# Kernel tuning notes

Measured on AMD Instinct MI355X. Metric: run time of the kernel, lower is better.

The kernel has to match this reference:

```python
import jax, jax.numpy as jnp
import numpy as np

H = 1024        # hidden_size
NH = 16         # num_attention_heads
HD = H // NH    # attention_head_size = 64
EPS = 1e-12


def setup_inputs() -> dict:
    key = jax.random.key(0)
    ks = jax.random.split(key, 12)
    B, S = 2, 2048
    s = 0.02
    return {
        "hidden_states": jax.random.normal(ks[0], (B, S, H), jnp.float32),
        "attention_mask": jnp.zeros((B, 1, 1, S), jnp.float32),
        "Wq": jax.random.normal(ks[1], (H, H), jnp.float32) * s,
        "bq": jnp.zeros((H,), jnp.float32),
        "Wk": jax.random.normal(ks[2], (H, H), jnp.float32) * s,
        "bk": jnp.zeros((H,), jnp.float32),
        "Wv": jax.random.normal(ks[3], (H, H), jnp.float32) * s,
        "bv": jnp.zeros((H,), jnp.float32),
        "Wd": jax.random.normal(ks[4], (H, H), jnp.float32) * s,
        "bd": jnp.zeros((H,), jnp.float32),
        "ln_gamma": jnp.ones((H,), jnp.float32),
        "ln_beta": jnp.zeros((H,), jnp.float32),
    }


def _split_heads(x):
    # [B,S,H] -> [B,NH,S,HD]
    B, S, _ = x.shape
    return x.reshape(B, S, NH, HD).transpose(0, 2, 1, 3)


def reference(hidden_states, attention_mask, Wq, bq, Wk, bk, Wv, bv, Wd, bd, ln_gamma, ln_beta):
    q = _split_heads(hidden_states @ Wq.T + bq)
    k = _split_heads(hidden_states @ Wk.T + bk)
    v = _split_heads(hidden_states @ Wv.T + bv)

    scores = jnp.einsum("bhqd,bhkd->bhqk", q, k) / jnp.sqrt(jnp.float32(HD))
    scores = scores + attention_mask
    probs = jax.nn.softmax(scores, axis=-1)  # attention dropout p=0

    ctx = jnp.einsum("bhqk,bhkd->bhqd", probs, v)
    B, _, S, _ = ctx.shape
    ctx = ctx.transpose(0, 2, 1, 3).reshape(B, S, H)

    proj = ctx @ Wd.T + bd  # output dropout p=0
    x = hidden_states + proj
    mu = jnp.mean(x, axis=-1, keepdims=True)
    var = jnp.mean(jnp.square(x - mu), axis=-1, keepdims=True)
    out = (x - mu) * jax.lax.rsqrt(var + EPS) * ln_gamma + ln_beta
    return out
```

## Files before the change

### kernel.cpp

```cpp
#include <hip/hip_runtime.h>

typedef unsigned short u16;
typedef unsigned int u32;
typedef __attribute__((ext_vector_type(4))) unsigned short u16x4;
typedef __attribute__((ext_vector_type(8))) unsigned short u16x8;
typedef __attribute__((ext_vector_type(8))) __bf16 bf16x8;
typedef __attribute__((ext_vector_type(4))) float f32x4;
typedef __attribute__((ext_vector_type(16))) float f32x16;
typedef __attribute__((ext_vector_type(2))) int i32x2;

#define S_LEN 2048
#define HDIM 1024
#define NHEAD 16
#define HD 64
#define MTOK 4096
#define QKV_STRIDE 4194304
#define LOG2E 1.44269504089f
#define QKSCL (0.125f * 1.44269504089f)

__device__ __forceinline__ float bf2f(u16 h) {
    unsigned u = ((unsigned)h) << 16;
    return __builtin_bit_cast(float, u);
}
__device__ __forceinline__ u16 f2bf(float f) {
    return __builtin_bit_cast(u16, (__bf16)f);
}
__device__ __forceinline__ bf16x8 as_bf16(u16x8 u) {
    union { u16x8 a; bf16x8 b; } c; c.a = u; return c.b;
}
__device__ __forceinline__ void gld_lds16(const u16* g, u16* l) {
    __builtin_amdgcn_global_load_lds((const __attribute__((address_space(1))) u16*)g,
                                     (__attribute__((address_space(3))) u16*)l, 16, 0, 0);
}

__device__ __forceinline__ void pl32swap(u32& a, u32& b) {
#if __has_builtin(__builtin_amdgcn_permlane32_swap)
    i32x2 r = __builtin_amdgcn_permlane32_swap((int)a, (int)b, false, false);
    a = (u32)r[0]; b = (u32)r[1];
#else
    u32 as = (u32)__shfl_xor((int)a, 32);
    u32 bs = (u32)__shfl_xor((int)b, 32);
    bool hi = (threadIdx.x & 32) != 0;
    u32 na = hi ? bs : a;
    u32 nb = hi ? b : as;
    a = na; b = nb;
#endif
}

__device__ __forceinline__ void cast4(const float* __restrict__ s, u16* __restrict__ d, int i) {
    f32x4 v = *(const f32x4*)(s + (size_t)i * 4);
    u16x4 o;
    o[0] = f2bf(v[0]); o[1] = f2bf(v[1]); o[2] = f2bf(v[2]); o[3] = f2bf(v[3]);
    *(u16x4*)(d + (size_t)i * 4) = o;
}

__global__ __launch_bounds__(256) void prep(const float* __restrict__ hs,
                                            const float* __restrict__ Wq, const float* __restrict__ Wk,
                                            const float* __restrict__ Wv, const float* __restrict__ Wd,
                                            const float* __restrict__ bq, const float* __restrict__ bk,
                                            const float* __restrict__ bv,
                                            u16* __restrict__ hsb, u16* __restrict__ wqkvb,
                                            u16* __restrict__ wdb, float* __restrict__ b3) {
    int bid = blockIdx.x, tid = threadIdx.x;
    if (bid < 4096) {
        cast4(hs, hsb, bid * 256 + tid);
    } else if (bid < 5120) {
        cast4(Wq, wqkvb, (bid - 4096) * 256 + tid);
    } else if (bid < 6144) {
        cast4(Wk, wqkvb + HDIM * HDIM, (bid - 5120) * 256 + tid);
    } else if (bid < 7168) {
        cast4(Wv, wqkvb + 2 * HDIM * HDIM, (bid - 6144) * 256 + tid);
    } else if (bid < 8192) {
        cast4(Wd, wdb, (bid - 7168) * 256 + tid);
    } else {
        int i = (bid - 8192) * 256 + tid;
        if (i < 3072) b3[i] = (i < 1024) ? bq[i] : (i < 2048) ? bk[i - 1024] : bv[i - 2048];
    }
}

__global__ __launch_bounds__(256, 3) void gemm_qkv(const u16* __restrict__ A, const u16* __restrict__ Bw,
                                                   const float* __restrict__ bias,
                                                   u16* __restrict__ outb, u16* __restrict__ vtout) {
    __shared__ alignas(16) u16 As[2][128 * 32];
    __shared__ alignas(16) u16 Bs[2][128 * 32];
    const int Kd = 1024;
    const int tid = threadIdx.x;
    const int wave = tid >> 6, lane = tid & 63;
    const int l15 = lane & 15, l4 = lane >> 4;
    const int m0 = blockIdx.y * 128, n0 = blockIdx.x * 128;
    const int wm = wave >> 1, wn = wave & 1;

    const int cc0 = wave * 2;
    const int srow = lane >> 2;
    const int sco = (lane & 3) * 8;

    f32x4 acc[4][4];
#pragma unroll
    for (int i = 0; i < 4; i++)
#pragma unroll
        for (int j = 0; j < 4; j++) acc[i][j] = (f32x4){0.f, 0.f, 0.f, 0.f};

    auto STAGE = [&](int k0, int buf) {
#pragma unroll
        for (int i = 0; i < 2; i++) {
            int cc = cc0 + i;
            int row = cc * 16 + srow;
            gld_lds16(A + (size_t)(m0 + row) * Kd + k0 + sco, &As[buf][cc * 512]);
            gld_lds16(Bw + (size_t)(n0 + row) * Kd + k0 + sco, &Bs[buf][cc * 512]);
        }
    };

    const int nt = Kd >> 5;
    STAGE(0, 0);
    for (int t = 0; t < nt; ++t) {
        __builtin_amdgcn_s_barrier();
        if (t + 1 < nt) {
            STAGE((t + 1) << 5, (t + 1) & 1);
            asm volatile("s_waitcnt vmcnt(4)" ::: "memory");
        } else {
            asm volatile("s_waitcnt vmcnt(0)" ::: "memory");
        }
        __builtin_amdgcn_s_barrier();
        const u16* as = &As[t & 1][0];
        const u16* bs = &Bs[t & 1][0];
        bf16x8 af[4], bf[4];
#pragma unroll
        for (int x = 0; x < 4; x++) {
            af[x] = as_bf16(*(const u16x8*)&as[(wm * 64 + x * 16 + l15) * 32 + l4 * 8]);
            bf[x] = as_bf16(*(const u16x8*)&bs[(wn * 64 + x * 16 + l15) * 32 + l4 * 8]);
        }
        __builtin_amdgcn_s_setprio(1);
#pragma unroll
        for (int mi = 0; mi < 4; mi++)
#pragma unroll
            for (int nj = 0; nj < 4; nj++)
                acc[mi][nj] = __builtin_amdgcn_mfma_f32_16x16x32_bf16(af[mi], bf[nj], acc[mi][nj], 0, 0, 0);
        __builtin_amdgcn_s_setprio(0);
    }

#pragma unroll
    for (int mi = 0; mi < 4; mi++) {
#pragma unroll
        for (int nj = 0; nj < 4; nj++) {
            int coln = n0 + wn * 64 + nj * 16 + l15;
            float bv_ = bias[coln];
            int rowb = m0 + wm * 64 + mi * 16 + l4 * 4;
            int which = coln >> 10, nn = coln & 1023;
            int hh = nn >> 6, dd = nn & 63;
            int bb = rowb >> 11, ss = rowb & 2047;
            if (which < 2) {
#pragma unroll
                for (int r = 0; r < 4; r++)
                    outb[(size_t)which * QKV_STRIDE + ((size_t)((bb << 4) + hh) * S_LEN + ss + r) * HD + dd] =
                        f2bf(acc[mi][nj][r] + bv_);
            } else {
                u16x4 o;
#pragma unroll
                for (int r = 0; r < 4; r++) o[r] = f2bf(acc[mi][nj][r] + bv_);
                *(u16x4*)(vtout + ((size_t)((bb << 4) + hh) * HD + dd) * S_LEN + ss) = o;
            }
        }
    }
}

__global__ __launch_bounds__(256, 3) void gemm_proj(const u16* __restrict__ A, const u16* __restrict__ Bw,
                                                    const float* __restrict__ bias,
                                                    u16* __restrict__ outb, int Nd, int Kd) {
    __shared__ alignas(16) u16 As[2][128 * 32];
    __shared__ alignas(16) u16 Bs[2][128 * 32];
    const int tid = threadIdx.x;
    const int wave = tid >> 6, lane = tid & 63;
    const int l15 = lane & 15, l4 = lane >> 4;
    const int m0 = blockIdx.y * 128, n0 = blockIdx.x * 128;
    const int wm = wave >> 1, wn = wave & 1;

    const int cc0 = wave * 2;
    const int srow = lane >> 2;
    const int sco = (lane & 3) * 8;

    f32x4 acc[4][4];
#pragma unroll
    for (int i = 0; i < 4; i++)
#pragma unroll
        for (int j = 0; j < 4; j++) acc[i][j] = (f32x4){0.f, 0.f, 0.f, 0.f};

    auto STAGE = [&](int k0, int buf) {
#pragma unroll
        for (int i = 0; i < 2; i++) {
            int cc = cc0 + i;
            int row = cc * 16 + srow;
            gld_lds16(A + (size_t)(m0 + row) * Kd + k0 + sco, &As[buf][cc * 512]);
            gld_lds16(Bw + (size_t)(n0 + row) * Kd + k0 + sco, &Bs[buf][cc * 512]);
        }
    };

    const int nt = Kd >> 5;
    STAGE(0, 0);
    for (int t = 0; t < nt; ++t) {
        __builtin_amdgcn_s_barrier();
        if (t + 1 < nt) {
            STAGE((t + 1) << 5, (t + 1) & 1);
            asm volatile("s_waitcnt vmcnt(4)" ::: "memory");
        } else {
            asm volatile("s_waitcnt vmcnt(0)" ::: "memory");
        }
        __builtin_amdgcn_s_barrier();
        const u16* as = &As[t & 1][0];
        const u16* bs = &Bs[t & 1][0];
        bf16x8 af[4], bf[4];
#pragma unroll
        for (int x = 0; x < 4; x++) {
            af[x] = as_bf16(*(const u16x8*)&as[(wm * 64 + x * 16 + l15) * 32 + l4 * 8]);
            bf[x] = as_bf16(*(const u16x8*)&bs[(wn * 64 + x * 16 + l15) * 32 + l4 * 8]);
        }
        __builtin_amdgcn_s_setprio(1);
#pragma unroll
        for (int mi = 0; mi < 4; mi++)
#pragma unroll
            for (int nj = 0; nj < 4; nj++)
                acc[mi][nj] = __builtin_amdgcn_mfma_f32_16x16x32_bf16(af[mi], bf[nj], acc[mi][nj], 0, 0, 0);
        __builtin_amdgcn_s_setprio(0);
    }

#pragma unroll
    for (int mi = 0; mi < 4; mi++) {
#pragma unroll
        for (int nj = 0; nj < 4; nj++) {
            int coln = n0 + wn * 64 + nj * 16 + l15;
            float bv_ = bias[coln];
            int rowb = m0 + wm * 64 + mi * 16 + l4 * 4;
#pragma unroll
            for (int r = 0; r < 4; r++)
                outb[(size_t)(rowb + r) * Nd + coln] = f2bf(acc[mi][nj][r] + bv_);
        }
    }
}

__global__ __launch_bounds__(512, 2) void flash_attn10(const u16* __restrict__ qkv,
                                                       const u16* __restrict__ vt,
                                                       const float* __restrict__ amask,
                                                       u16* __restrict__ ctx) {
    __shared__ alignas(16) char smem[102400];

    const int tid = threadIdx.x;
    const int wave = tid >> 6, lane = tid & 63;
    const int l31 = lane & 31;
    const int hi = lane >> 5;
    const int hi4 = hi * 4;
    const int g = wave >> 2;
    const int ws = wave & 3;

    const int lid = blockIdx.x;
    const int idx = lid >> 3;
    const int bh = (lid & 7) * 4 + (idx >> 3);
    const int qb = idx & 7;
    const int b = bh >> 4, h = bh & 15;
    const int qr0 = qb * 256 + ws * 64;

    const u16* qh = qkv + (size_t)bh * (S_LEN * HD);
    const u16* kh = qh + QKV_STRIDE;
    const u16* vth = vt + (size_t)bh * (S_LEN * HD);

    u16* Mlb = (u16*)(smem + 98304);

    {
        f32x4 m = *(const f32x4*)(amask + (size_t)b * S_LEN + tid * 4);
        u16x4 mm;
#pragma unroll
        for (int j = 0; j < 4; j++) mm[j] = f2bf(m[j] * LOG2E);
        *(u16x4*)&Mlb[tid * 4] = mm;
    }

    bf16x8 qf0[4], qf1[4];
#pragma unroll
    for (int s = 0; s < 4; ++s) {
        qf0[s] = as_bf16(*(const u16x8*)(qh + (size_t)(qr0 + l31) * HD + s * 16 + hi * 8));
        qf1[s] = as_bf16(*(const u16x8*)(qh + (size_t)(qr0 + 32 + l31) * HD + s * 16 + hi * 8));
    }

    __syncthreads();

    const int srow = lane >> 3;
    const int schunk = (lane & 7) ^ srow;
    const u16* kss = kh + (size_t)(g * 1024 + ws * 16 + srow) * HD + schunk * 8;
    const u16* vss = vth + (size_t)(ws * 16 + srow) * S_LEN + g * 1024 + schunk * 8;

    f32x16 oacc00, oacc01, oacc10, oacc11;
#pragma unroll
    for (int i = 0; i < 16; ++i) { oacc00[i] = 0.f; oacc01[i] = 0.f; oacc10[i] = 0.f; oacc11[i] = 0.f; }
    float l_run0 = 0.f, l_run1 = 0.f;

    auto STAGE = [&](int t, int buf) {
        u16* base = (u16*)(smem + g * 49152 + buf * 16384);
        u16* kd = base + ws * 1024;
        u16* vd = base + 4096 + ws * 1024;
        const u16* ks = kss + (size_t)t * 64 * HD;
        const u16* vs = vss + t * 64;
        gld_lds16(ks, kd);
        gld_lds16(ks + 8 * HD, kd + 512);
        gld_lds16(vs, vd);
        gld_lds16(vs + 8 * S_LEN, vd + 512);
    };

    auto tile = [&](int t, int buf) {
        const u16* kb = (const u16*)(smem + g * 49152 + buf * 16384);
        const u16* vb = kb + 4096;
        const int kv0 = g * 1024 + t * 64;
#pragma unroll
        for (int sub = 0; sub < 2; ++sub) {
            f32x16 acc0, acc1;
#pragma unroll
            for (int i = 0; i < 16; ++i) { acc0[i] = 0.f; acc1[i] = 0.f; }
            const int kvrow = sub * 32 + l31;
            const int ksw = (kvrow & 7) << 3;
            __builtin_amdgcn_s_setprio(1);
#pragma unroll
            for (int s = 0; s < 4; ++s) {
                bf16x8 kf = as_bf16(*(const u16x8*)&kb[kvrow * 64 + (((s * 2 + hi) << 3) ^ ksw)]);
                acc0 = __builtin_amdgcn_mfma_f32_32x32x16_bf16(kf, qf0[s], acc0, 0, 0, 0);
                acc1 = __builtin_amdgcn_mfma_f32_32x32x16_bf16(kf, qf1[s], acc1, 0, 0, 0);
            }
            __builtin_amdgcn_s_setprio(0);
            u32 pw0[8], pw1[8];
#pragma unroll
            for (int rg = 0; rg < 4; ++rg) {
                u16x4 mraw = *(const u16x4*)&Mlb[kv0 + sub * 32 + rg * 8 + hi4];
#pragma unroll
                for (int r2 = 0; r2 < 2; ++r2) {
                    float m0 = bf2f(mraw[r2 * 2]), m1 = bf2f(mraw[r2 * 2 + 1]);
                    float pa0 = __builtin_amdgcn_exp2f(acc0[rg * 4 + r2 * 2] * QKSCL + m0);
                    float pb0 = __builtin_amdgcn_exp2f(acc0[rg * 4 + r2 * 2 + 1] * QKSCL + m1);
                    float pa1 = __builtin_amdgcn_exp2f(acc1[rg * 4 + r2 * 2] * QKSCL + m0);
                    float pb1 = __builtin_amdgcn_exp2f(acc1[rg * 4 + r2 * 2 + 1] * QKSCL + m1);
                    l_run0 += pa0 + pb0;
                    l_run1 += pa1 + pb1;
                    pw0[rg * 2 + r2] = (u32)f2bf(pa0) | ((u32)f2bf(pb0) << 16);
                    pw1[rg * 2 + r2] = (u32)f2bf(pa1) | ((u32)f2bf(pb1) << 16);
                }
            }
            pl32swap(pw0[0], pw0[2]); pl32swap(pw0[1], pw0[3]);
            pl32swap(pw0[4], pw0[6]); pl32swap(pw0[5], pw0[7]);
            pl32swap(pw1[0], pw1[2]); pl32swap(pw1[1], pw1[3]);
            pl32swap(pw1[4], pw1[6]); pl32swap(pw1[5], pw1[7]);
            union { u32 w[4]; u16x8 v; } u0a, u0b, u1a, u1b;
            u0a.w[0] = pw0[0]; u0a.w[1] = pw0[1]; u0a.w[2] = pw0[2]; u0a.w[3] = pw0[3];
            u0b.w[0] = pw0[4]; u0b.w[1] = pw0[5]; u0b.w[2] = pw0[6]; u0b.w[3] = pw0[7];
            u1a.w[0] = pw1[0]; u1a.w[1] = pw1[1]; u1a.w[2] = pw1[2]; u1a.w[3] = pw1[3];
            u1b.w[0] = pw1[4]; u1b.w[1] = pw1[5]; u1b.w[2] = pw1[6]; u1b.w[3] = pw1[7];
            bf16x8 pf0a = as_bf16(u0a.v), pf0b = as_bf16(u0b.v);
            bf16x8 pf1a = as_bf16(u1a.v), pf1b = as_bf16(u1b.v);
            __builtin_amdgcn_s_setprio(1);
            {
                const int drow0 = l31, dsw0 = (drow0 & 7) << 3;
                const int drow1 = 32 + l31, dsw1 = (drow1 & 7) << 3;
                const int c0 = (sub * 4 + hi) << 3;
                const int c1 = ((sub * 2 + 1) * 2 + hi) << 3;
                bf16x8 vf;
                vf = as_bf16(*(const u16x8*)&vb[drow0 * 64 + (c0 ^ dsw0)]);
                oacc00 = __builtin_amdgcn_mfma_f32_32x32x16_bf16(vf, pf0a, oacc00, 0, 0, 0);
                oacc10 = __builtin_amdgcn_mfma_f32_32x32x16_bf16(vf, pf1a, oacc10, 0, 0, 0);
                vf = as_bf16(*(const u16x8*)&vb[drow0 * 64 + (c1 ^ dsw0)]);
                oacc00 = __builtin_amdgcn_mfma_f32_32x32x16_bf16(vf, pf0b, oacc00, 0, 0, 0);
                oacc10 = __builtin_amdgcn_mfma_f32_32x32x16_bf16(vf, pf1b, oacc10, 0, 0, 0);
                vf = as_bf16(*(const u16x8*)&vb[drow1 * 64 + (c0 ^ dsw1)]);
                oacc01 = __builtin_amdgcn_mfma_f32_32x32x16_bf16(vf, pf0a, oacc01, 0, 0, 0);
                oacc11 = __builtin_amdgcn_mfma_f32_32x32x16_bf16(vf, pf1a, oacc11, 0, 0, 0);
                vf = as_bf16(*(const u16x8*)&vb[drow1 * 64 + (c1 ^ dsw1)]);
                oacc01 = __builtin_amdgcn_mfma_f32_32x32x16_bf16(vf, pf0b, oacc01, 0, 0, 0);
                oacc11 = __builtin_amdgcn_mfma_f32_32x32x16_bf16(vf, pf1b, oacc11, 0, 0, 0);
            }
            __builtin_amdgcn_s_setprio(0);
        }
    };

    STAGE(0, 0);
    STAGE(1, 1);
    for (int t = 0; t < 16; ++t) {
        if (t < 15) {
            asm volatile("s_waitcnt vmcnt(4)" ::: "memory");
        } else {
            asm volatile("s_waitcnt vmcnt(0)" ::: "memory");
        }
        __builtin_amdgcn_s_barrier();
        if (t + 2 < 16) STAGE(t + 2, (t + 2) % 3);
        tile(t, t % 3);
    }

    float l0 = l_run0 + __shfl_xor(l_run0, 32);
    float l1 = l_run1 + __shfl_xor(l_run1, 32);
    __syncthreads();
    float* Oex = (float*)smem;
    float* lsum = (float*)(smem + 65536);
    if (g == 1) {
#pragma unroll
        for (int rg = 0; rg < 4; ++rg)
#pragma unroll
            for (int rr = 0; rr < 4; ++rr) {
                int dA = hi4 + 8 * rg + rr;
                int dB = 32 + hi4 + 8 * rg + rr;
                Oex[ws * 4096 + dA * 64 + l31]      = oacc00[rg * 4 + rr];
                Oex[ws * 4096 + dB * 64 + l31]      = oacc01[rg * 4 + rr];
                Oex[ws * 4096 + dA * 64 + 32 + l31] = oacc10[rg * 4 + rr];
                Oex[ws * 4096 + dB * 64 + 32 + l31] = oacc11[rg * 4 + rr];
            }
        if (lane < 32) { lsum[ws * 64 + l31] = l0; lsum[ws * 64 + 32 + l31] = l1; }
    }
    __syncthreads();
    if (g == 0) {
        float inv0 = 1.0f / (l0 + lsum[ws * 64 + l31]);
        float inv1 = 1.0f / (l1 + lsum[ws * 64 + 32 + l31]);
        u16* cp0 = ctx + ((size_t)b * S_LEN + qr0 + l31) * HDIM + h * HD;
        u16* cp1 = ctx + ((size_t)b * S_LEN + qr0 + 32 + l31) * HDIM + h * HD;
#pragma unroll
        for (int rg = 0; rg < 4; ++rg) {
            u16x4 oA0, oB0, oA1, oB1;
#pragma unroll
            for (int rr = 0; rr < 4; ++rr) {
                int dA = hi4 + 8 * rg + rr;
                int dB = 32 + hi4 + 8 * rg + rr;
                oA0[rr] = f2bf((oacc00[rg * 4 + rr] + Oex[ws * 4096 + dA * 64 + l31]) * inv0);
                oB0[rr] = f2bf((oacc01[rg * 4 + rr] + Oex[ws * 4096 + dB * 64 + l31]) * inv0);
                oA1[rr] = f2bf((oacc10[rg * 4 + rr] + Oex[ws * 4096 + dA * 64 + 32 + l31]) * inv1);
                oB1[rr] = f2bf((oacc11[rg * 4 + rr] + Oex[ws * 4096 + dB * 64 + 32 + l31]) * inv1);
            }
            *(u16x4*)(cp0 + hi4 + 8 * rg) = oA0;
            *(u16x4*)(cp0 + 32 + hi4 + 8 * rg) = oB0;
            *(u16x4*)(cp1 + hi4 + 8 * rg) = oA1;
            *(u16x4*)(cp1 + 32 + hi4 + 8 * rg) = oB1;
        }
    }
}

__global__ __launch_bounds__(256) void resid_ln(const float* __restrict__ hs, const u16* __restrict__ proj,
                                                const float* __restrict__ g, const float* __restrict__ be,
                                                float* __restrict__ out) {
    int row = blockIdx.x, tid = threadIdx.x;
    int base = row * HDIM + tid * 4;
    f32x4 a = *(const f32x4*)(hs + base);
    u16x4 pb = *(const u16x4*)(proj + base);
    f32x4 x;
#pragma unroll
    for (int j = 0; j < 4; j++) x[j] = a[j] + bf2f(pb[j]);
    float s = x[0] + x[1] + x[2] + x[3];
    float sq = x[0] * x[0] + x[1] * x[1] + x[2] * x[2] + x[3] * x[3];
#pragma unroll
    for (int m = 1; m < 64; m <<= 1) {
        s += __shfl_xor(s, m);
        sq += __shfl_xor(sq, m);
    }
    __shared__ float red[8];
    int wave = tid >> 6, lane = tid & 63;
    if (lane == 0) { red[wave] = s; red[4 + wave] = sq; }
    __syncthreads();
    s = red[0] + red[1] + red[2] + red[3];
    sq = red[4] + red[5] + red[6] + red[7];
    float mean = s * (1.0f / 1024.0f);
    float var = sq * (1.0f / 1024.0f) - mean * mean;
    float rstd = rsqrtf(fmaxf(var, 0.f) + 1e-12f);
    f32x4 gg = *(const f32x4*)(g + tid * 4);
    f32x4 bb = *(const f32x4*)(be + tid * 4);
    f32x4 o;
#pragma unroll
    for (int j = 0; j < 4; j++) o[j] = (x[j] - mean) * rstd * gg[j] + bb[j];
    *(f32x4*)(out + base) = o;
}

extern "C" void kernel_launch(void* const* d_in, const int* in_sizes, int n_in,
                              void* d_out, int out_size, void* d_ws, size_t ws_size,
                              hipStream_t stream) {
    const float* hs    = (const float*)d_in[0];
    const float* amask = (const float*)d_in[1];
    const float* Wq    = (const float*)d_in[2];
    const float* bq    = (const float*)d_in[3];
    const float* Wk    = (const float*)d_in[4];
    const float* bk    = (const float*)d_in[5];
    const float* Wv    = (const float*)d_in[6];
    const float* bv    = (const float*)d_in[7];
    const float* Wd    = (const float*)d_in[8];
    const float* bd    = (const float*)d_in[9];
    const float* gamma = (const float*)d_in[10];
    const float* beta  = (const float*)d_in[11];

    char* ws = (char*)d_ws;
    u16*   hsb   = (u16*)(ws);
    u16*   Wqkvb = (u16*)(ws + ((size_t)8 << 20));
    u16*   Wdb   = (u16*)(ws + ((size_t)14 << 20));
    u16*   qkv   = (u16*)(ws + ((size_t)16 << 20));
    u16*   vt    = qkv + 2 * (size_t)QKV_STRIDE;
    u16*   ctx   = (u16*)(ws + ((size_t)40 << 20));
    u16*   projb = (u16*)(ws + ((size_t)48 << 20));
    float* b3    = (float*)(ws + ((size_t)64 << 20));

    prep<<<8204, 256, 0, stream>>>(hs, Wq, Wk, Wv, Wd, bq, bk, bv, hsb, Wqkvb, Wdb, b3);

    gemm_qkv<<<dim3(24, 32), 256, 0, stream>>>(hsb, Wqkvb, b3, qkv, vt);

    flash_attn10<<<256, 512, 0, stream>>>(qkv, vt, amask, ctx);

    gemm_proj<<<dim3(8, 32), 256, 0, stream>>>(ctx, Wdb, bd, projb, HDIM, HDIM);

    resid_ln<<<MTOK, 256, 0, stream>>>(hs, projb, gamma, beta, (float*)d_out);
}
```

Baseline: 125.4 us.

## Give each wave private double-buffered K/V tiles and drop block barriers

The attention kernel stops sharing K/V tiles across the four waves of a group. Each wave now loads its own 32-row K/V tiles into a private double buffer, which removes the block-wide barrier from the main loop; synchronisation becomes per-wave waitcnt. The cost is four times the K/V global/LDS traffic and 132KB of LDS, which caps the kernel at one 512-thread block per CU (launch bounds changed from 2 to 1). The hidden part of the kernel after the loop still uses smem offsets from the old layout, so that region may need checking.

```diff
diff --git a/kernel.cpp b/kernel.cpp
--- a/kernel.cpp
+++ b/kernel.cpp
@@ -236,11 +236,12 @@
     }
 }
 
-__global__ __launch_bounds__(512, 2) void flash_attn10(const u16* __restrict__ qkv,
+__global__ __launch_bounds__(512, 1) void flash_attn12(const u16* __restrict__ qkv,
                                                        const u16* __restrict__ vt,
                                                        const float* __restrict__ amask,
                                                        u16* __restrict__ ctx) {
-    __shared__ alignas(16) char smem[102400];
+    __shared__ alignas(16) char smem[135168];
+    u16* smem16 = (u16*)smem;
 
     const int tid = threadIdx.x;
     const int wave = tid >> 6, lane = tid & 63;
@@ -261,7 +262,7 @@
     const u16* kh = qh + QKV_STRIDE;
     const u16* vth = vt + (size_t)bh * (S_LEN * HD);
 
-    u16* Mlb = (u16*)(smem + 98304);
+    u16* Mlb = smem16 + 65536;
 
     {
         f32x4 m = *(const f32x4*)(amask + (size_t)b * S_LEN + tid * 4);
@@ -280,10 +281,12 @@
 
     __syncthreads();
 
-    const int srow = lane >> 3;
-    const int schunk = (lane & 7) ^ srow;
-    const u16* kss = kh + (size_t)(g * 1024 + ws * 16 + srow) * HD + schunk * 8;
-    const u16* vss = vth + (size_t)(ws * 16 + srow) * S_LEN + g * 1024 + schunk * 8;
+    u16* wbase = smem16 + wave * 8192;
+
+    const int ksc8 = ((lane & 7) ^ (lane >> 3)) * 8;
+    const u16* kss = kh + (size_t)(g * 1024 + (lane >> 3)) * HD + ksc8;
+    const int vsc8 = ((lane & 3) ^ ((lane >> 2) & 3)) * 8;
+    const u16* vss = vth + (size_t)(lane >> 2) * S_LEN + g * 1024 + vsc8;
 
     f32x16 oacc00, oacc01, oacc10, oacc11;
 #pragma unroll
@@ -291,99 +294,97 @@
     float l_run0 = 0.f, l_run1 = 0.f;
 
     auto STAGE = [&](int t, int buf) {
-        u16* base = (u16*)(smem + g * 49152 + buf * 16384);
-        u16* kd = base + ws * 1024;
-        u16* vd = base + 4096 + ws * 1024;
-        const u16* ks = kss + (size_t)t * 64 * HD;
-        const u16* vs = vss + t * 64;
-        gld_lds16(ks, kd);
-        gld_lds16(ks + 8 * HD, kd + 512);
-        gld_lds16(vs, vd);
-        gld_lds16(vs + 8 * S_LEN, vd + 512);
+        u16* kd = wbase + buf * 4096;
+        u16* vd = kd + 2048;
+        const u16* ks = kss + (size_t)t * 32 * HD;
+        const u16* vs = vss + t * 32;
+#pragma unroll
+        for (int j = 0; j < 4; ++j)
+            gld_lds16(ks + (size_t)j * 8 * HD, kd + j * 512);
+#pragma unroll
+        for (int j = 0; j < 4; ++j)
+            gld_lds16(vs + (size_t)j * 16 * S_LEN, vd + j * 512);
     };
 
     auto tile = [&](int t, int buf) {
-        const u16* kb = (const u16*)(smem + g * 49152 + buf * 16384);
-        const u16* vb = kb + 4096;
-        const int kv0 = g * 1024 + t * 64;
-#pragma unroll
-        for (int sub = 0; sub < 2; ++sub) {
-            f32x16 acc0, acc1;
-#pragma unroll
-            for (int i = 0; i < 16; ++i) { acc0[i] = 0.f; acc1[i] = 0.f; }
-            const int kvrow = sub * 32 + l31;
-            const int ksw = (kvrow & 7) << 3;
-            __builtin_amdgcn_s_setprio(1);
-#pragma unroll
-            for (int s = 0; s < 4; ++s) {
-                bf16x8 kf = as_bf16(*(const u16x8*)&kb[kvrow * 64 + (((s * 2 + hi) << 3) ^ ksw)]);
-                acc0 = __builtin_amdgcn_mfma_f32_32x32x16_bf16(kf, qf0[s], acc0, 0, 0, 0);
-                acc1 = __builtin_amdgcn_mfma_f32_32x32x16_bf16(kf, qf1[s], acc1, 0, 0, 0);
+        const u16* kb = wbase + buf * 4096;
+        const u16* vb = kb + 2048;
+        const int kv0 = g * 1024 + t * 32;
+        f32x16 acc0, acc1;
+#pragma unroll
+        for (int i = 0; i < 16; ++i) { acc0[i] = 0.f; acc1[i] = 0.f; }
+        const int ksw = (l31 & 7) << 3;
+        __builtin_amdgcn_s_setprio(1);
+#pragma unroll
+        for (int s = 0; s < 4; ++s) {
+            bf16x8 kf = as_bf16(*(const u16x8*)&kb[l31 * 64 + ((((s * 2 + hi) << 3)) ^ ksw)]);
+            acc0 = __builtin_amdgcn_mfma_f32_32x32x16_bf16(kf, qf0[s], acc0, 0, 0, 0);
+            acc1 = __builtin_amdgcn_mfma_f32_32x32x16_bf16(kf, qf1[s], acc1, 0, 0, 0);
+        }
+        __builtin_amdgcn_s_setprio(0);
+        u32 pw0[8], pw1[8];
+#pragma unroll
+        for (int rg = 0; rg < 4; ++rg) {
+            u16x4 mraw = *(const u16x4*)&Mlb[kv0 + rg * 8 + hi4];
+#pragma unroll
+            for (int r2 = 0; r2 < 2; ++r2) {
+                float m0 = bf2f(mraw[r2 * 2]), m1 = bf2f(mraw[r2 * 2 + 1]);
+                float pa0 = __builtin_amdgcn_exp2f(acc0[rg * 4 + r2 * 2] * QKSCL + m0);
+                float pb0 = __builtin_amdgcn_exp2f(acc0[rg * 4 + r2 * 2 + 1] * QKSCL + m1);
+                float pa1 = __builtin_amdgcn_exp2f(acc1[rg * 4 + r2 * 2] * QKSCL + m0);
+                float pb1 = __builtin_amdgcn_exp2f(acc1[rg * 4 + r2 * 2 + 1] * QKSCL + m1);
+                l_run0 += pa0 + pb0;
+                l_run1 += pa1 + pb1;
+                pw0[rg * 2 + r2] = (u32)f2bf(pa0) | ((u32)f2bf(pb0) << 16);
+                pw1[rg * 2 + r2] = (u32)f2bf(pa1) | ((u32)f2bf(pb1) << 16);
             }
-            __builtin_amdgcn_s_setprio(0);
-            u32 pw0[8], pw1[8];
-#pragma unroll
-            for (int rg = 0; rg < 4; ++rg) {
-                u16x4 mraw = *(const u16x4*)&Mlb[kv0 + sub * 32 + rg * 8 + hi4];
-#pragma unroll
-                for (int r2 = 0; r2 < 2; ++r2) {
-                    float m0 = bf2f(mraw[r2 * 2]), m1 = bf2f(mraw[r2 * 2 + 1]);
-                    float pa0 = __builtin_amdgcn_exp2f(acc0[rg * 4 + r2 * 2] * QKSCL + m0);
-                    float pb0 = __builtin_amdgcn_exp2f(acc0[rg * 4 + r2 * 2 + 1] * QKSCL + m1);
-                    float pa1 = __builtin_amdgcn_exp2f(acc1[rg * 4 + r2 * 2] * QKSCL + m0);
-                    float pb1 = __builtin_amdgcn_exp2f(acc1[rg * 4 + r2 * 2 + 1] * QKSCL + m1);
-                    l_run0 += pa0 + pb0;
-                    l_run1 += pa1 + pb1;
-                    pw0[rg * 2 + r2] = (u32)f2bf(pa0) | ((u32)f2bf(pb0) << 16);
-                    pw1[rg * 2 + r2] = (u32)f2bf(pa1) | ((u32)f2bf(pb1) << 16);
-                }
-            }
-            pl32swap(pw0[0], pw0[2]); pl32swap(pw0[1], pw0[3]);
-            pl32swap(pw0[4], pw0[6]); pl32swap(pw0[5], pw0[7]);
-            pl32swap(pw1[0], pw1[2]); pl32swap(pw1[1], pw1[3]);
-            pl32swap(pw1[4], pw1[6]); pl32swap(pw1[5], pw1[7]);
-            union { u32 w[4]; u16x8 v; } u0a, u0b, u1a, u1b;
-            u0a.w[0] = pw0[0]; u0a.w[1] = pw0[1]; u0a.w[2] = pw0[2]; u0a.w[3] = pw0[3];
-            u0b.w[0] = pw0[4]; u0b.w[1] = pw0[5]; u0b.w[2] = pw0[6]; u0b.w[3] = pw0[7];
-            u1a.w[0] = pw1[0]; u1a.w[1] = pw1[1]; u1a.w[2] = pw1[2]; u1a.w[3] = pw1[3];
-            u1b.w[0] = pw1[4]; u1b.w[1] = pw1[5]; u1b.w[2] = pw1[6]; u1b.w[3] = pw1[7];
-            bf16x8 pf0a = as_bf16(u0a.v), pf0b = as_bf16(u0b.v);
-            bf16x8 pf1a = as_bf16(u1a.v), pf1b = as_bf16(u1b.v);
-            __builtin_amdgcn_s_setprio(1);
-            {
-                const int drow0 = l31, dsw0 = (drow0 & 7) << 3;
-                const int drow1 = 32 + l31, dsw1 = (drow1 & 7) << 3;
-                const int c0 = (sub * 4 + hi) << 3;
-                const int c1 = ((sub * 2 + 1) * 2 + hi) << 3;
-                bf16x8 vf;
-                vf = as_bf16(*(const u16x8*)&vb[drow0 * 64 + (c0 ^ dsw0)]);
-                oacc00 = __builtin_amdgcn_mfma_f32_32x32x16_bf16(vf, pf0a, oacc00, 0, 0, 0);
-                oacc10 = __builtin_amdgcn_mfma_f32_32x32x16_bf16(vf, pf1a, oacc10, 0, 0, 0);
-                vf = as_bf16(*(const u16x8*)&vb[drow0 * 64 + (c1 ^ dsw0)]);
-                oacc00 = __builtin_amdgcn_mfma_f32_32x32x16_bf16(vf, pf0b, oacc00, 0, 0, 0);
-                oacc10 = __builtin_amdgcn_mfma_f32_32x32x16_bf16(vf, pf1b, oacc10, 0, 0, 0);
-                vf = as_bf16(*(const u16x8*)&vb[drow1 * 64 + (c0 ^ dsw1)]);
-                oacc01 = __builtin_amdgcn_mfma_f32_32x32x16_bf16(vf, pf0a, oacc01, 0, 0, 0);
-                oacc11 = __builtin_amdgcn_mfma_f32_32x32x16_bf16(vf, pf1a, oacc11, 0, 0, 0);
-                vf = as_bf16(*(const u16x8*)&vb[drow1 * 64 + (c1 ^ dsw1)]);
-                oacc01 = __builtin_amdgcn_mfma_f32_32x32x16_bf16(vf, pf0b, oacc01, 0, 0, 0);
-                oacc11 = __builtin_amdgcn_mfma_f32_32x32x16_bf16(vf, pf1b, oacc11, 0, 0, 0);
-            }
-            __builtin_amdgcn_s_setprio(0);
-        }
+        }
+        pl32swap(pw0[0], pw0[2]); pl32swap(pw0[1], pw0[3]);
+        pl32swap(pw0[4], pw0[6]); pl32swap(pw0[5], pw0[7]);
+        pl32swap(pw1[0], pw1[2]); pl32swap(pw1[1], pw1[3]);
+        pl32swap(pw1[4], pw1[6]); pl32swap(pw1[5], pw1[7]);
+        union { u32 w[4]; u16x8 v; } u0a, u0b, u1a, u1b;
+        u0a.w[0] = pw0[0]; u0a.w[1] = pw0[1]; u0a.w[2] = pw0[2]; u0a.w[3] = pw0[3];
+        u0b.w[0] = pw0[4]; u0b.w[1] = pw0[5]; u0b.w[2] = pw0[6]; u0b.w[3] = pw0[7];
+        u1a.w[0] = pw1[0]; u1a.w[1] = pw1[1]; u1a.w[2] = pw1[2]; u1a.w[3] = pw1[3];
+        u1b.w[0] = pw1[4]; u1b.w[1] = pw1[5]; u1b.w[2] = pw1[6]; u1b.w[3] = pw1[7];
+        bf16x8 pf0a = as_bf16(u0a.v), pf0b = as_bf16(u0b.v);
+        bf16x8 pf1a = as_bf16(u1a.v), pf1b = as_bf16(u1b.v);
+        __builtin_amdgcn_s_setprio(1);
+        {
+            const int dr0 = l31, sw0 = dr0 & 3;
+            const int dr1 = 32 + l31, sw1 = dr1 & 3;
+            bf16x8 vf;
+            vf = as_bf16(*(const u16x8*)&vb[dr0 * 32 + ((hi ^ sw0) << 3)]);
+            oacc00 = __builtin_amdgcn_mfma_f32_32x32x16_bf16(vf, pf0a, oacc00, 0, 0, 0);
+            oacc10 = __builtin_amdgcn_mfma_f32_32x32x16_bf16(vf, pf1a, oacc10, 0, 0, 0);
+            vf = as_bf16(*(const u16x8*)&vb[dr0 * 32 + (((2 + hi) ^ sw0) << 3)]);
+            oacc00 = __builtin_amdgcn_mfma_f32_32x32x16_bf16(vf, pf0b, oacc00, 0, 0, 0);
+            oacc10 = __builtin_amdgcn_mfma_f32_32x32x16_bf16(vf, pf1b, oacc10, 0, 0, 0);
+            vf = as_bf16(*(const u16x8*)&vb[dr1 * 32 + ((hi ^ sw1) << 3)]);
+            oacc01 = __builtin_amdgcn_mfma_f32_32x32x16_bf16(vf, pf0a, oacc01, 0, 0, 0);
+            oacc11 = __builtin_amdgcn_mfma_f32_32x32x16_bf16(vf, pf1a, oacc11, 0, 0, 0);
+            vf = as_bf16(*(const u16x8*)&vb[dr1 * 32 + (((2 + hi) ^ sw1) << 3)]);
+            oacc01 = __builtin_amdgcn_mfma_f32_32x32x16_bf16(vf, pf0b, oacc01, 0, 0, 0);
+            oacc11 = __builtin_amdgcn_mfma_f32_32x32x16_bf16(vf, pf1b, oacc11, 0, 0, 0);
+        }
+        __builtin_amdgcn_s_setprio(0);
     };
 
     STAGE(0, 0);
     STAGE(1, 1);
-    for (int t = 0; t < 16; ++t) {
-        if (t < 15) {
-            asm volatile("s_waitcnt vmcnt(4)" ::: "memory");
+    for (int t = 0; t < 32; ++t) {
+        if (t < 31) {
+            asm volatile("s_waitcnt vmcnt(8)" ::: "memory");
         } else {
             asm volatile("s_waitcnt vmcnt(0)" ::: "memory");
         }
-        __builtin_amdgcn_s_barrier();
-        if (t + 2 < 16) STAGE(t + 2, (t + 2) % 3);
-        tile(t, t % 3);
+        tile(t, t & 1);
+        if (t + 2 < 32) {
+            asm volatile("s_waitcnt lgkmcnt(0)" ::: "memory");
+            __builtin_amdgcn_sched_barrier(0);
+            STAGE(t + 2, t & 1);
+        }
     }
 
     float l0 = l_run0 + __shfl_xor(l_run0, 32);
@@ -495,7 +496,7 @@
 
     gemm_qkv<<<dim3(24, 32), 256, 0, stream>>>(hsb, Wqkvb, b3, qkv, vt);
 
-    flash_attn10<<<256, 512, 0, stream>>>(qkv, vt, amask, ctx);
+    flash_attn12<<<256, 512, 0, stream>>>(qkv, vt, amask, ctx);
 
     gemm_proj<<<dim3(8, 32), 256, 0, stream>>>(ctx, Wdb, bd, projb, HDIM, HDIM);
 
```

After: 131.0 us. 1.04x slower.
